# Performance work log

Hardware: AMD Instinct MI355X
Metric: run time of the kernel (lower is better)

The kernel has to match this reference:

```python
import jax, jax.numpy as jnp
import numpy as np

K = 8       # branching factor == L (max child positions)
DEPTH = 6   # tree depth
NTREE = 2   # number of trees in the forest
C = 8       # hidden states
MSYM = 32   # output symbols
NGEN = 16   # parallel generative models


def _build_tree():
    starts = [(K ** d - 1) // (K - 1) for d in range(DEPTH + 2)]
    Nt = starts[DEPTH + 1]
    N = NTREE * Nt
    rng = np.random.default_rng(0)
    x = rng.integers(0, MSYM, size=N).astype(np.int32)
    local = np.arange(Nt)
    pos = np.tile(np.where(local == 0, 0, (local - 1) % K).astype(np.int32), NTREE)
    batch = np.repeat(np.arange(NTREE), Nt).astype(np.int32)
    levels = {}
    for d in range(1, DEPTH + 1):
        ch = np.concatenate([t * Nt + np.arange(starts[d], starts[d + 1]) for t in range(NTREE)]).astype(np.int32)
        upa = np.concatenate([t * Nt + np.arange(starts[d - 1], starts[d]) for t in range(NTREE)]).astype(np.int32)
        levels[d] = (ch, upa)
    return x, pos, batch, levels


def setup_inputs() -> dict:
    key = jax.random.key(0)
    kA, kB, kPi, kSP = jax.random.split(key, 4)
    x, pos, batch, levels = _build_tree()
    inp = {
        'A': jax.random.normal(kA, (C, C, K, NGEN), jnp.float32) * 2.5,
        'B': jax.random.normal(kB, (C, MSYM, NGEN), jnp.float32) * 2.5,
        'Pi': jax.random.normal(kPi, (C, K, NGEN), jnp.float32) * 2.5,
        'SP': jax.random.normal(kSP, (K, NGEN), jnp.float32) * 2.5,
        'x': jnp.asarray(x),
        'pos': jnp.asarray(pos),
        'batch': jnp.asarray(batch),
        'leaves': jnp.asarray(levels[DEPTH][0]),
    }
    for d in range(1, DEPTH + 1):
        inp[f'ch{d}'] = jnp.asarray(levels[d][0])
        inp[f'upa{d}'] = jnp.asarray(levels[d][1])
    return inp


def _upward(A, B, Pi, SP, x, pos, batch, leaves, levels):
    # softmax reparameterization (matches the per-generator per-position loops)
    smA = jax.nn.softmax(A, axis=0)    # over parent state
    smB = jax.nn.softmax(B, axis=1)    # over symbols
    smPi = jax.nn.softmax(Pi, axis=0)  # over states
    smSP = jax.nn.softmax(SP, axis=0)  # over positions

    N = x.shape[0]
    beta = jnp.zeros((N, C, NGEN), smA.dtype)
    ll = jnp.zeros((N, NGEN), smA.dtype)

    # leaves: beta = Pi[:, pos] * B[:, x], normalized per node
    b_leaf = jnp.transpose(smPi[:, pos[leaves]], (1, 0, 2)) * jnp.transpose(smB[:, x[leaves]], (1, 0, 2))  # (nl,C,G)
    nu = b_leaf.sum(1)
    beta = beta.at[leaves].set(b_leaf / nu[:, None])
    ll = ll.at[leaves].set(jnp.log(nu))

    # per-position transition weighted by position prior: (L, i_parent, j_child, G)
    Mmat = smSP[:, None, None, :] * jnp.transpose(smA, (2, 0, 1, 3))

    # upward over levels, deepest first; children of each parent are contiguous
    # with column index == child position, so scatter-add == reshape + einsum
    for ch, upa in reversed(levels):
        U = upa.shape[0]
        bch = beta[ch].reshape(U, K, C, NGEN)              # (U, pos, C_child, G)
        tb = jnp.einsum('uljg,lijg->uig', bch, Mmat)       # t_beta at parents
        bl = tb * jnp.transpose(smB[:, x[upa]], (1, 0, 2)) # (U, C, G)
        nu = bl.sum(1)
        beta = beta.at[upa].set(bl / nu[:, None])
        ll = ll.at[upa].set(jnp.log(nu))

    # sum per-node log scaling factors over each tree
    return jax.ops.segment_sum(ll, batch, num_segments=NTREE)


def reference(A, B, Pi, SP, x, pos, batch, leaves, ch1, upa1, ch2, upa2, ch3, upa3, ch4, upa4, ch5, upa5, ch6, upa6):
    levels = [(ch1, upa1), (ch2, upa2), (ch3, upa3), (ch4, upa4), (ch5, upa5), (ch6, upa6)]
    return _upward(A, B, Pi, SP, x, pos, batch, leaves, levels)
```

## Files before the change

kernel.cpp:

```cpp
#include <hip/hip_runtime.h>


constexpr int NT_NODES = 299593;
constexpr int S0 = 0, S1 = 1, S2 = 9, S3 = 73, S4 = 585, S5 = 4681, S6 = 37449;

__device__ __forceinline__ unsigned bfbits(float x) {
    unsigned v = __float_as_uint(x);
    return (v + 0x7fffu + ((v >> 16) & 1u)) >> 16;
}

__device__ __forceinline__ float sel8(const float v[8], bool c0, bool c1, bool c2) {
    float a0 = c0 ? v[1] : v[0];
    float a1 = c0 ? v[3] : v[2];
    float a2 = c0 ? v[5] : v[4];
    float a3 = c0 ? v[7] : v[6];
    float b0 = c1 ? a1 : a0;
    float b1 = c1 ? a3 : a2;
    return c2 ? b1 : b0;
}

__global__ __launch_bounds__(256) void xpack(
    const int* __restrict__ x, uint4* __restrict__ rec)
{
    int pidx = blockIdx.x * 256 + threadIdx.x;
    int t = pidx >> 15, localP = pidx & 32767;
    const int base = t * NT_NODES;
    const int xb = base + S6 + localP * 8;
    unsigned d0 = 0, d1 = 0;
    #pragma unroll
    for (int l = 0; l < 4; ++l) d0 |= ((unsigned)x[xb + l]) << (8 * l);
    #pragma unroll
    for (int l = 0; l < 4; ++l) d1 |= ((unsigned)x[xb + 4 + l]) << (8 * l);
    unsigned xm = (unsigned)x[base + S5 + localP];
    unsigned xr = (unsigned)x[base + S4 + (localP >> 3)];
    unsigned x3 = (unsigned)x[base + S3 + (localP >> 6)];
    rec[pidx] = make_uint4(d0, d1, xm | (xr << 8) | (x3 << 16), 0u);
}

__global__ __launch_bounds__(256) void stage0T(
    const float* __restrict__ A, const float* __restrict__ B,
    const float* __restrict__ Pi, const float* __restrict__ SP,
    float* __restrict__ MtN, float* __restrict__ smBtN,
    unsigned* __restrict__ Tp, unsigned* __restrict__ EMp)
{
    int g = blockIdx.x;
    int tid = threadIdx.x;
    __shared__ __align__(16) float mL[512];
    __shared__ __align__(16) float bLs[256];
    __shared__ __align__(16) float piLs[64];

    float sp[8];
    {
        float mx = -1e30f;
        #pragma unroll
        for (int l = 0; l < 8; ++l) { sp[l] = SP[l * 16 + g]; mx = fmaxf(mx, sp[l]); }
        float s = 0.f;
        #pragma unroll
        for (int l = 0; l < 8; ++l) { sp[l] = __expf(sp[l] - mx); s += sp[l]; }
        float r = 1.f / s;
        #pragma unroll
        for (int l = 0; l < 8; ++l) sp[l] *= r;
    }

    if (tid < 64) {
        int j = tid & 7, l = tid >> 3;
        float a[8]; float mx = -1e30f;
        #pragma unroll
        for (int i = 0; i < 8; ++i) { a[i] = A[((i * 8 + j) * 8 + l) * 16 + g]; mx = fmaxf(mx, a[i]); }
        float s = 0.f;
        #pragma unroll
        for (int i = 0; i < 8; ++i) { a[i] = __expf(a[i] - mx); s += a[i]; }
        float scale = sp[l] / s;
        #pragma unroll
        for (int i = 0; i < 8; ++i) {
            float m = a[i] * scale;
            mL[(l * 8 + j) * 8 + i] = m;
            MtN[((g * 8 + l) * 8 + j) * 8 + i] = m;
        }
    } else if (tid < 72) {
        int c = tid - 64;
        float vv[32]; float mx = -1e30f;
        #pragma unroll
        for (int m = 0; m < 32; ++m) { vv[m] = B[(c * 32 + m) * 16 + g]; mx = fmaxf(mx, vv[m]); }
        float s = 0.f;
        #pragma unroll
        for (int m = 0; m < 32; ++m) { vv[m] = __expf(vv[m] - mx); s += vv[m]; }
        float r = 1.f / s;
        #pragma unroll
        for (int m = 0; m < 32; ++m) {
            float p = vv[m] * r;
            bLs[m * 8 + c] = p;
            smBtN[(g * 32 + m) * 8 + c] = p;
        }
    } else if (tid < 80) {
        int l = tid - 72;
        float a[8]; float mx = -1e30f;
        #pragma unroll
        for (int c = 0; c < 8; ++c) { a[c] = Pi[(c * 8 + l) * 16 + g]; mx = fmaxf(mx, a[c]); }
        float s = 0.f;
        #pragma unroll
        for (int c = 0; c < 8; ++c) { a[c] = __expf(a[c] - mx); s += a[c]; }
        float r = 1.f / s;
        #pragma unroll
        for (int c = 0; c < 8; ++c) piLs[l * 8 + c] = a[c] * r;
    }
    __syncthreads();

    {
        int m = tid & 31, l = tid >> 5;
        float pb[8]; float w = 0.f;
        #pragma unroll
        for (int c = 0; c < 8; ++c) { pb[c] = piLs[l * 8 + c] * bLs[m * 8 + c]; w += pb[c]; }
        float rw = 1.f / w;
        float t[8];
        #pragma unroll
        for (int i = 0; i < 8; ++i) t[i] = 0.f;
        #pragma unroll
        for (int c = 0; c < 8; ++c) {
            float p = pb[c];
            #pragma unroll
            for (int i = 0; i < 8; ++i) t[i] = fmaf(p, mL[(l * 8 + c) * 8 + i], t[i]);
        }
        #pragma unroll
        for (int k = 0; k < 4; ++k) {
            unsigned lo = bfbits(t[2 * k] * rw), hi = bfbits(t[2 * k + 1] * rw);
            Tp[(g * 5 + k) * 256 + tid] = lo | (hi << 16);
        }
        Tp[(g * 5 + 4) * 256 + tid] = __float_as_uint(__logf(w));
    }
    if (tid < 32) {
        #pragma unroll
        for (int k = 0; k < 4; ++k) {
            unsigned lo = bfbits(bLs[tid * 8 + 2 * k]), hi = bfbits(bLs[tid * 8 + 2 * k + 1]);
            EMp[(g * 4 + k) * 32 + tid] = lo | (hi << 16);
        }
    }
}

__global__ __launch_bounds__(256, 2) void upleaf(
    const float* __restrict__ MtN, const unsigned* __restrict__ Tp,
    const unsigned* __restrict__ EMp, const uint4* __restrict__ rec,
    float* __restrict__ lv3,
    float* __restrict__ llout)
{
    __shared__ unsigned TL[256 * 5 + 32 * 5];
    __shared__ float b4[256 * 9];
    __shared__ float llp[4];

    int bid = blockIdx.x;
    int g = bid & 15;
    int pg = bid >> 4;
    int tid = threadIdx.x;
    int wave = tid >> 6;
    int lane = tid & 63;
    int gu = __builtin_amdgcn_readfirstlane(g);
    int s = pg * 256 + tid;
    int t = (s >= 4096) ? 1 : 0;
    int localS = s - t * 4096;

    #pragma unroll
    for (int k = 0; k < 5; ++k)
        TL[tid * 5 + k] = Tp[(gu * 5 + k) * 256 + tid];
    if (tid < 32) {
        #pragma unroll
        for (int k = 0; k < 4; ++k)
            TL[1280 + tid * 5 + k] = EMp[(gu * 4 + k) * 32 + tid];
    }

    uint4 rc[8];
    {
        const uint4* rp = rec + ((size_t)t * 32768 + (size_t)localS * 8);
        #pragma unroll
        for (int u = 0; u < 8; ++u) rc[u] = rp[u];
    }
    int xr = (rc[0].z >> 8) & 255;
    int x3 = (rc[0].z >> 16) & 255;
    __syncthreads();

    float ll = 0.f;
    float bm[64];

    #pragma unroll
    for (int u = 0; u < 8; ++u) {
        int xl[8];
        xl[0] = rc[u].x & 255; xl[1] = (rc[u].x >> 8) & 255;
        xl[2] = (rc[u].x >> 16) & 255; xl[3] = rc[u].x >> 24;
        xl[4] = rc[u].y & 255; xl[5] = (rc[u].y >> 8) & 255;
        xl[6] = (rc[u].y >> 16) & 255; xl[7] = rc[u].y >> 24;
        int xm = rc[u].z & 255;

        float pa[8] = {0.f, 0.f, 0.f, 0.f, 0.f, 0.f, 0.f, 0.f};
        #pragma unroll
        for (int l = 0; l < 8; ++l) {
            int r5 = (l * 32 + xl[l]) * 5;
            unsigned u0 = TL[r5], u1 = TL[r5 + 1], u2 = TL[r5 + 2], u3 = TL[r5 + 3];
            ll += __uint_as_float(TL[r5 + 4]);
            pa[0] += __uint_as_float(u0 << 16); pa[1] += __uint_as_float(u0 & 0xffff0000u);
            pa[2] += __uint_as_float(u1 << 16); pa[3] += __uint_as_float(u1 & 0xffff0000u);
            pa[4] += __uint_as_float(u2 << 16); pa[5] += __uint_as_float(u2 & 0xffff0000u);
            pa[6] += __uint_as_float(u3 << 16); pa[7] += __uint_as_float(u3 & 0xffff0000u);
        }
        int e5 = 1280 + xm * 5;
        unsigned e0 = TL[e5], e1 = TL[e5 + 1], e2 = TL[e5 + 2], e3 = TL[e5 + 3];
        pa[0] *= __uint_as_float(e0 << 16); pa[1] *= __uint_as_float(e0 & 0xffff0000u);
        pa[2] *= __uint_as_float(e1 << 16); pa[3] *= __uint_as_float(e1 & 0xffff0000u);
        pa[4] *= __uint_as_float(e2 << 16); pa[5] *= __uint_as_float(e2 & 0xffff0000u);
        pa[6] *= __uint_as_float(e3 << 16); pa[7] *= __uint_as_float(e3 & 0xffff0000u);
        float nu = ((pa[0] + pa[1]) + (pa[2] + pa[3])) + ((pa[4] + pa[5]) + (pa[6] + pa[7]));
        ll += __logf(nu);
        float rn = __builtin_amdgcn_rcpf(nu);
        #pragma unroll
        for (int c = 0; c < 8; ++c) bm[u * 8 + c] = pa[c] * rn;
    }

    {
        float pr[8] = {0.f, 0.f, 0.f, 0.f, 0.f, 0.f, 0.f, 0.f};
        const float* Mg = MtN + (gu << 9);
        #pragma unroll
        for (int k = 0; k < 64; ++k) {
            float b = bm[k];
            #pragma unroll
            for (int i = 0; i < 8; ++i) pr[i] = fmaf(b, Mg[k * 8 + i], pr[i]);
        }
        int e5 = 1280 + xr * 5;
        unsigned e0 = TL[e5], e1 = TL[e5 + 1], e2 = TL[e5 + 2], e3 = TL[e5 + 3];
        pr[0] *= __uint_as_float(e0 << 16); pr[1] *= __uint_as_float(e0 & 0xffff0000u);
        pr[2] *= __uint_as_float(e1 << 16); pr[3] *= __uint_as_float(e1 & 0xffff0000u);
        pr[4] *= __uint_as_float(e2 << 16); pr[5] *= __uint_as_float(e2 & 0xffff0000u);
        pr[6] *= __uint_as_float(e3 << 16); pr[7] *= __uint_as_float(e3 & 0xffff0000u);
        float nur = ((pr[0] + pr[1]) + (pr[2] + pr[3])) + ((pr[4] + pr[5]) + (pr[6] + pr[7]));
        ll += __logf(nur);
        float rr = __builtin_amdgcn_rcpf(nur);
        #pragma unroll
        for (int c = 0; c < 8; ++c) b4[tid * 9 + c] = pr[c] * rr;
    }
    __syncthreads();

    {
        int o = tid >> 3, j = tid & 7;
        int s3 = pg * 32 + o;
        int t3 = (s3 >= 512) ? 1 : 0;
        float bch[8];
        #pragma unroll
        for (int l = 0; l < 8; ++l) bch[l] = b4[(o * 8 + l) * 9 + j];
        float pr[8] = {0.f, 0.f, 0.f, 0.f, 0.f, 0.f, 0.f, 0.f};
        #pragma unroll
        for (int l = 0; l < 8; ++l) {
            const float4* mp = (const float4*)(MtN + (gu << 9) + (l << 6) + (j << 3));
            float4 m0 = mp[0], m1 = mp[1];
            float b = bch[l];
            pr[0] = fmaf(b, m0.x, pr[0]); pr[1] = fmaf(b, m0.y, pr[1]);
            pr[2] = fmaf(b, m0.z, pr[2]); pr[3] = fmaf(b, m0.w, pr[3]);
            pr[4] = fmaf(b, m1.x, pr[4]); pr[5] = fmaf(b, m1.y, pr[5]);
            pr[6] = fmaf(b, m1.z, pr[6]); pr[7] = fmaf(b, m1.w, pr[7]);
        }
        #pragma unroll
        for (int m = 1; m <= 4; m <<= 1) {
            #pragma unroll
            for (int i = 0; i < 8; ++i) pr[i] += __shfl_xor(pr[i], m);
        }
        int xn = __shfl(x3, o * 8);
        int e5 = 1280 + xn * 5;
        unsigned e0 = TL[e5], e1 = TL[e5 + 1], e2 = TL[e5 + 2], e3 = TL[e5 + 3];
        pr[0] *= __uint_as_float(e0 << 16); pr[1] *= __uint_as_float(e0 & 0xffff0000u);
        pr[2] *= __uint_as_float(e1 << 16); pr[3] *= __uint_as_float(e1 & 0xffff0000u);
        pr[4] *= __uint_as_float(e2 << 16); pr[5] *= __uint_as_float(e2 & 0xffff0000u);
        pr[6] *= __uint_as_float(e3 << 16); pr[7] *= __uint_as_float(e3 & 0xffff0000u);
        float nur = ((pr[0] + pr[1]) + (pr[2] + pr[3])) + ((pr[4] + pr[5]) + (pr[6] + pr[7]));
        float rr = __builtin_amdgcn_rcpf(nur);
        if (j == 0) {
            ll += __logf(nur);
            float4* dp = (float4*)(lv3 + ((size_t)g * 1024 + s3) * 8);
            dp[0] = make_float4(pr[0] * rr, pr[1] * rr, pr[2] * rr, pr[3] * rr);
            dp[1] = make_float4(pr[4] * rr, pr[5] * rr, pr[6] * rr, pr[7] * rr);
        }
    }

    #pragma unroll
    for (int m = 1; m < 64; m <<= 1) ll += __shfl_xor(ll, m);
    if (lane == 0) llp[wave] = ll;
    __syncthreads();
    if (tid == 0) llout[gu * 32 + pg] = (llp[0] + llp[1]) + (llp[2] + llp[3]);
}

__global__ __launch_bounds__(256) void uptop(
    const float* __restrict__ MtN, const float* __restrict__ smBtN,
    const int* __restrict__ x,
    const float* __restrict__ lv3,
    const float* __restrict__ ll1,
    float* __restrict__ out)
{
    int g = blockIdx.x;
    int tid = threadIdx.x;
    __shared__ __align__(16) float bet2[128 * 8];
    __shared__ __align__(16) float bet1[16 * 8];
    __shared__ float redA[256], redB[256];

    float ll0 = 0.f, llt1 = 0.f;
    if (tid < 32) {
        float v = ll1[g * 32 + tid];
        if (tid < 16) ll0 = v; else llt1 = v;
    }

    const float* Mg = MtN + (g << 9);

    if (tid < 128) {
        int t = tid >> 6, n2 = tid & 63;
        float bch[64];
        const float4* sp = (const float4*)(lv3 + ((size_t)g * 1024 + t * 512 + n2 * 8) * 8);
        #pragma unroll
        for (int v = 0; v < 16; ++v) {
            float4 f = sp[v];
            bch[4 * v + 0] = f.x; bch[4 * v + 1] = f.y;
            bch[4 * v + 2] = f.z; bch[4 * v + 3] = f.w;
        }
        float pa[8] = {0.f, 0.f, 0.f, 0.f, 0.f, 0.f, 0.f, 0.f};
        #pragma unroll
        for (int k = 0; k < 64; ++k) {
            float b = bch[k];
            #pragma unroll
            for (int i = 0; i < 8; ++i) pa[i] = fmaf(b, Mg[k * 8 + i], pa[i]);
        }
        int x2 = x[t * NT_NODES + S2 + n2];
        const float4* ep = (const float4*)(smBtN + ((g << 5) + x2) * 8);
        float4 e0 = ep[0], e1 = ep[1];
        pa[0] *= e0.x; pa[1] *= e0.y; pa[2] *= e0.z; pa[3] *= e0.w;
        pa[4] *= e1.x; pa[5] *= e1.y; pa[6] *= e1.z; pa[7] *= e1.w;
        float nu = ((pa[0] + pa[1]) + (pa[2] + pa[3])) + ((pa[4] + pa[5]) + (pa[6] + pa[7]));
        float lg = __logf(nu);
        if (t == 0) ll0 += lg; else llt1 += lg;
        float rn = __builtin_amdgcn_rcpf(nu);
        float4* dp = (float4*)(bet2 + tid * 8);
        dp[0] = make_float4(pa[0] * rn, pa[1] * rn, pa[2] * rn, pa[3] * rn);
        dp[1] = make_float4(pa[4] * rn, pa[5] * rn, pa[6] * rn, pa[7] * rn);
    }
    __syncthreads();

    if (tid < 128) {
        int o = tid >> 3, j = tid & 7;
        int t = o >> 3, n1 = o & 7;
        bool c0 = (j & 1) != 0, c1 = (j & 2) != 0, c2 = (j & 4) != 0;
        float bch[8];
        #pragma unroll
        for (int l = 0; l < 8; ++l) bch[l] = bet2[(t * 64 + n1 * 8 + l) * 8 + j];
        float pr[8] = {0.f, 0.f, 0.f, 0.f, 0.f, 0.f, 0.f, 0.f};
        #pragma unroll
        for (int l = 0; l < 8; ++l) {
            const float4* mp = (const float4*)(MtN + (g << 9) + (l << 6) + (j << 3));
            float4 m0 = mp[0], m1 = mp[1];
            float b = bch[l];
            pr[0] = fmaf(b, m0.x, pr[0]); pr[1] = fmaf(b, m0.y, pr[1]);
            pr[2] = fmaf(b, m0.z, pr[2]); pr[3] = fmaf(b, m0.w, pr[3]);
            pr[4] = fmaf(b, m1.x, pr[4]); pr[5] = fmaf(b, m1.y, pr[5]);
            pr[6] = fmaf(b, m1.z, pr[6]); pr[7] = fmaf(b, m1.w, pr[7]);
        }
        #pragma unroll
        for (int m = 1; m <= 4; m <<= 1) {
            #pragma unroll
            for (int i = 0; i < 8; ++i) pr[i] += __shfl_xor(pr[i], m);
        }
        int x1 = x[t * NT_NODES + S1 + n1];
        const float4* ep = (const float4*)(smBtN + ((g << 5) + x1) * 8);
        float4 e0 = ep[0], e1 = ep[1];
        pr[0] *= e0.x; pr[1] *= e0.y; pr[2] *= e0.z; pr[3] *= e0.w;
        pr[4] *= e1.x; pr[5] *= e1.y; pr[6] *= e1.z; pr[7] *= e1.w;
        float nu = ((pr[0] + pr[1]) + (pr[2] + pr[3])) + ((pr[4] + pr[5]) + (pr[6] + pr[7]));
        if (j == 0) { float lg = __logf(nu); if (t == 0) ll0 += lg; else llt1 += lg; }
        float rn = __builtin_amdgcn_rcpf(nu);
        bet1[o * 8 + j] = sel8(pr, c0, c1, c2) * rn;
    }
    __syncthreads();

    if (tid < 16) {
        int t = tid >> 3, j = tid & 7;
        float bch[8];
        #pragma unroll
        for (int l = 0; l < 8; ++l) bch[l] = bet1[(t * 8 + l) * 8 + j];
        float pr[8] = {0.f, 0.f, 0.f, 0.f, 0.f, 0.f, 0.f, 0.f};
        #pragma unroll
        for (int l = 0; l < 8; ++l) {
            const float4* mp = (const float4*)(MtN + (g << 9) + (l << 6) + (j << 3));
            float4 m0 = mp[0], m1 = mp[1];
            float b = bch[l];
            pr[0] = fmaf(b, m0.x, pr[0]); pr[1] = fmaf(b, m0.y, pr[1]);
            pr[2] = fmaf(b, m0.z, pr[2]); pr[3] = fmaf(b, m0.w, pr[3]);
            pr[4] = fmaf(b, m1.x, pr[4]); pr[5] = fmaf(b, m1.y, pr[5]);
            pr[6] = fmaf(b, m1.z, pr[6]); pr[7] = fmaf(b, m1.w, pr[7]);
        }
        #pragma unroll
        for (int m = 1; m <= 4; m <<= 1) {
            #pragma unroll
            for (int i = 0; i < 8; ++i) pr[i] += __shfl_xor(pr[i], m);
        }
        int x0 = x[t * NT_NODES + S0];
        const float4* ep = (const float4*)(smBtN + ((g << 5) + x0) * 8);
        float4 e0 = ep[0], e1 = ep[1];
        pr[0] *= e0.x; pr[1] *= e0.y; pr[2] *= e0.z; pr[3] *= e0.w;
        pr[4] *= e1.x; pr[5] *= e1.y; pr[6] *= e1.z; pr[7] *= e1.w;
        float nu = ((pr[0] + pr[1]) + (pr[2] + pr[3])) + ((pr[4] + pr[5]) + (pr[6] + pr[7]));
        if (j == 0) { float lg = __logf(nu); if (t == 0) ll0 += lg; else llt1 += lg; }
    }

    redA[tid] = ll0; redB[tid] = llt1;
    __syncthreads();
    for (int step = 128; step > 0; step >>= 1) {
        if (tid < step) { redA[tid] += redA[tid + step]; redB[tid] += redB[tid + step]; }
        __syncthreads();
    }
    if (tid == 0) { out[g] = redA[0]; out[16 + g] = redB[0]; }
}

extern "C" void kernel_launch(void* const* d_in, const int* in_sizes, int n_in,
                              void* d_out, int out_size, void* d_ws, size_t ws_size,
                              hipStream_t stream)
{
    const float* A  = (const float*)d_in[0];
    const float* B  = (const float*)d_in[1];
    const float* Pi = (const float*)d_in[2];
    const float* SP = (const float*)d_in[3];
    const int*   x  = (const int*)d_in[4];

    float* ws     = (float*)d_ws;
    float* MtN    = ws;
    float* smBtN  = MtN + 8192;
    unsigned* Tp  = (unsigned*)(smBtN + 4096);
    unsigned* EMp = Tp + 20480;
    uint4* rec    = (uint4*)(EMp + 2048);
    float* lv3    = (float*)(rec + 65536);
    float* ll1    = lv3 + 131072;
    float* out    = (float*)d_out;

    stage0T<<<16, 256, 0, stream>>>(A, B, Pi, SP, MtN, smBtN, Tp, EMp);
    xpack<<<256, 256, 0, stream>>>(x, rec);
    upleaf<<<512, 256, 0, stream>>>(MtN, Tp, EMp, rec, lv3, ll1);
    uptop<<<16, 256, 0, stream>>>(MtN, smBtN, x, lv3, ll1, out);
}
```

Before: 30.66 us.

## Merge prep kernels and split level-5 work across wave pairs in upleaf

The parameter-softmax kernel and the symbol-packing kernel are fused into one launch, with block index selecting the role, which removes one kernel launch. In upleaf each level-5 parent's eight children are now split across two waves, with partial sums combined through shared memory. This halves per-thread register arrays, raises the occupancy hint to 4 blocks per CU and doubles the grid to 1024 blocks. In exchange it adds an extra barrier and shared-memory exchange, leaves half the threads idle during the level-4 step, and doubles the number of partial log-likelihoods that uptop must read.

```diff
diff --git a/kernel.cpp b/kernel.cpp
--- a/kernel.cpp
+++ b/kernel.cpp
@@ -19,32 +19,35 @@
     return c2 ? b1 : b0;
 }
 
-__global__ __launch_bounds__(256) void xpack(
-    const int* __restrict__ x, uint4* __restrict__ rec)
-{
-    int pidx = blockIdx.x * 256 + threadIdx.x;
-    int t = pidx >> 15, localP = pidx & 32767;
-    const int base = t * NT_NODES;
-    const int xb = base + S6 + localP * 8;
-    unsigned d0 = 0, d1 = 0;
-    #pragma unroll
-    for (int l = 0; l < 4; ++l) d0 |= ((unsigned)x[xb + l]) << (8 * l);
-    #pragma unroll
-    for (int l = 0; l < 4; ++l) d1 |= ((unsigned)x[xb + 4 + l]) << (8 * l);
-    unsigned xm = (unsigned)x[base + S5 + localP];
-    unsigned xr = (unsigned)x[base + S4 + (localP >> 3)];
-    unsigned x3 = (unsigned)x[base + S3 + (localP >> 6)];
-    rec[pidx] = make_uint4(d0, d1, xm | (xr << 8) | (x3 << 16), 0u);
-}
-
-__global__ __launch_bounds__(256) void stage0T(
+__global__ __launch_bounds__(256) void prep(
     const float* __restrict__ A, const float* __restrict__ B,
     const float* __restrict__ Pi, const float* __restrict__ SP,
+    const int* __restrict__ x,
     float* __restrict__ MtN, float* __restrict__ smBtN,
-    unsigned* __restrict__ Tp, unsigned* __restrict__ EMp)
+    unsigned* __restrict__ Tp, unsigned* __restrict__ EMp,
+    uint4* __restrict__ rec)
 {
-    int g = blockIdx.x;
+    int bid = blockIdx.x;
     int tid = threadIdx.x;
+
+    if (bid >= 16) {
+        int pidx = (bid - 16) * 256 + tid;
+        int t = pidx >> 15, localP = pidx & 32767;
+        const int base = t * NT_NODES;
+        const int xb = base + S6 + localP * 8;
+        unsigned d0 = 0, d1 = 0;
+        #pragma unroll
+        for (int l = 0; l < 4; ++l) d0 |= ((unsigned)x[xb + l]) << (8 * l);
+        #pragma unroll
+        for (int l = 0; l < 4; ++l) d1 |= ((unsigned)x[xb + 4 + l]) << (8 * l);
+        unsigned xm = (unsigned)x[base + S5 + localP];
+        unsigned xr = (unsigned)x[base + S4 + (localP >> 3)];
+        unsigned x3 = (unsigned)x[base + S3 + (localP >> 6)];
+        rec[pidx] = make_uint4(d0, d1, xm | (xr << 8) | (x3 << 16), 0u);
+        return;
+    }
+
+    int g = bid;
     __shared__ __align__(16) float mL[512];
     __shared__ __align__(16) float bLs[256];
     __shared__ __align__(16) float piLs[64];
@@ -137,14 +140,14 @@
     }
 }
 
-__global__ __launch_bounds__(256, 2) void upleaf(
+__global__ __launch_bounds__(256, 4) void upleaf(
     const float* __restrict__ MtN, const unsigned* __restrict__ Tp,
     const unsigned* __restrict__ EMp, const uint4* __restrict__ rec,
     float* __restrict__ lv3,
     float* __restrict__ llout)
 {
     __shared__ unsigned TL[256 * 5 + 32 * 5];
-    __shared__ float b4[256 * 9];
+    __shared__ float ex[128 * 9];
     __shared__ float llp[4];
 
     int bid = blockIdx.x;
@@ -153,8 +156,11 @@
     int tid = threadIdx.x;
     int wave = tid >> 6;
     int lane = tid & 63;
+    int half = wave & 1;
+    int pairIdx = wave >> 1;
     int gu = __builtin_amdgcn_readfirstlane(g);
-    int s = pg * 256 + tid;
+    int idx = pairIdx * 64 + lane;
+    int s = pg * 128 + idx;
     int t = (s >= 4096) ? 1 : 0;
     int localS = s - t * 4096;
 
@@ -167,21 +173,22 @@
             TL[1280 + tid * 5 + k] = EMp[(gu * 4 + k) * 32 + tid];
     }
 
-    uint4 rc[8];
+    uint4 rc[4];
     {
-        const uint4* rp = rec + ((size_t)t * 32768 + (size_t)localS * 8);
-        #pragma unroll
-        for (int u = 0; u < 8; ++u) rc[u] = rp[u];
-    }
-    int xr = (rc[0].z >> 8) & 255;
-    int x3 = (rc[0].z >> 16) & 255;
+        const uint4* rp = rec + ((size_t)t * 32768 + (size_t)localS * 8 + half * 4);
+        #pragma unroll
+        for (int u = 0; u < 4; ++u) rc[u] = rp[u];
+    }
+    unsigned meta = rc[0].z;
+    int xr = (meta >> 8) & 255;
+    unsigned x3b = (meta >> 16) & 255;
     __syncthreads();
 
     float ll = 0.f;
-    float bm[64];
+    float bm[32];
 
     #pragma unroll
-    for (int u = 0; u < 8; ++u) {
+    for (int u = 0; u < 4; ++u) {
         int xl[8];
         xl[0] = rc[u].x & 255; xl[1] = (rc[u].x >> 8) & 255;
         xl[2] = (rc[u].x >> 16) & 255; xl[3] = rc[u].x >> 24;
@@ -213,66 +220,76 @@
         for (int c = 0; c < 8; ++c) bm[u * 8 + c] = pa[c] * rn;
     }
 
+    float pr[8] = {0.f, 0.f, 0.f, 0.f, 0.f, 0.f, 0.f, 0.f};
     {
-        float pr[8] = {0.f, 0.f, 0.f, 0.f, 0.f, 0.f, 0.f, 0.f};
-        const float* Mg = MtN + (gu << 9);
-        #pragma unroll
-        for (int k = 0; k < 64; ++k) {
+        const float* Mg = MtN + (gu << 9) + (half << 8);
+        #pragma unroll
+        for (int k = 0; k < 32; ++k) {
             float b = bm[k];
             #pragma unroll
             for (int i = 0; i < 8; ++i) pr[i] = fmaf(b, Mg[k * 8 + i], pr[i]);
         }
+    }
+    if (half) {
+        #pragma unroll
+        for (int c = 0; c < 8; ++c) ex[idx * 9 + c] = pr[c];
+    }
+    __syncthreads();
+    if (!half) {
+        float tot[8];
+        #pragma unroll
+        for (int c = 0; c < 8; ++c) tot[c] = pr[c] + ex[idx * 9 + c];
         int e5 = 1280 + xr * 5;
         unsigned e0 = TL[e5], e1 = TL[e5 + 1], e2 = TL[e5 + 2], e3 = TL[e5 + 3];
-        pr[0] *= __uint_as_float(e0 << 16); pr[1] *= __uint_as_float(e0 & 0xffff0000u);
-        pr[2] *= __uint_as_float(e1 << 16); pr[3] *= __uint_as_float(e1 & 0xffff0000u);
-        pr[4] *= __uint_as_float(e2 << 16); pr[5] *= __uint_as_float(e2 & 0xffff0000u);
-        pr[6] *= __uint_as_float(e3 << 16); pr[7] *= __uint_as_float(e3 & 0xffff0000u);
-        float nur = ((pr[0] + pr[1]) + (pr[2] + pr[3])) + ((pr[4] + pr[5]) + (pr[6] + pr[7]));
+        tot[0] *= __uint_as_float(e0 << 16); tot[1] *= __uint_as_float(e0 & 0xffff0000u);
+        tot[2] *= __uint_as_float(e1 << 16); tot[3] *= __uint_as_float(e1 & 0xffff0000u);
+        tot[4] *= __uint_as_float(e2 << 16); tot[5] *= __uint_as_float(e2 & 0xffff0000u);
+        tot[6] *= __uint_as_float(e3 << 16); tot[7] *= __uint_as_float(e3 & 0xffff0000u);
+        float nur = ((tot[0] + tot[1]) + (tot[2] + tot[3])) + ((tot[4] + tot[5]) + (tot[6] + tot[7]));
         ll += __logf(nur);
         float rr = __builtin_amdgcn_rcpf(nur);
         #pragma unroll
-        for (int c = 0; c < 8; ++c) b4[tid * 9 + c] = pr[c] * rr;
-    }
-    __syncthreads();
-
-    {
+        for (int c = 0; c < 8; ++c) ex[idx * 9 + c] = tot[c] * rr;
+        ex[idx * 9 + 8] = __uint_as_float(x3b);
+    }
+    __syncthreads();
+
+    if (tid < 128) {
         int o = tid >> 3, j = tid & 7;
-        int s3 = pg * 32 + o;
-        int t3 = (s3 >= 512) ? 1 : 0;
+        int s3 = pg * 16 + o;
         float bch[8];
         #pragma unroll
-        for (int l = 0; l < 8; ++l) bch[l] = b4[(o * 8 + l) * 9 + j];
-        float pr[8] = {0.f, 0.f, 0.f, 0.f, 0.f, 0.f, 0.f, 0.f};
+        for (int l = 0; l < 8; ++l) bch[l] = ex[(o * 8 + l) * 9 + j];
+        float pr3[8] = {0.f, 0.f, 0.f, 0.f, 0.f, 0.f, 0.f, 0.f};
         #pragma unroll
         for (int l = 0; l < 8; ++l) {
             const float4* mp = (const float4*)(MtN + (gu << 9) + (l << 6) + (j << 3));
             float4 m0 = mp[0], m1 = mp[1];
             float b = bch[l];
-            pr[0] = fmaf(b, m0.x, pr[0]); pr[1] = fmaf(b, m0.y, pr[1]);
-            pr[2] = fmaf(b, m0.z, pr[2]); pr[3] = fmaf(b, m0.w, pr[3]);
-            pr[4] = fmaf(b, m1.x, pr[4]); pr[5] = fmaf(b, m1.y, pr[5]);
-            pr[6] = fmaf(b, m1.z, pr[6]); pr[7] = fmaf(b, m1.w, pr[7]);
+            pr3[0] = fmaf(b, m0.x, pr3[0]); pr3[1] = fmaf(b, m0.y, pr3[1]);
+            pr3[2] = fmaf(b, m0.z, pr3[2]); pr3[3] = fmaf(b, m0.w, pr3[3]);
+            pr3[4] = fmaf(b, m1.x, pr3[4]); pr3[5] = fmaf(b, m1.y, pr3[5]);
+            pr3[6] = fmaf(b, m1.z, pr3[6]); pr3[7] = fmaf(b, m1.w, pr3[7]);
         }
         #pragma unroll
         for (int m = 1; m <= 4; m <<= 1) {
             #pragma unroll
-            for (int i = 0; i < 8; ++i) pr[i] += __shfl_xor(pr[i], m);
-        }
-        int xn = __shfl(x3, o * 8);
+            for (int i = 0; i < 8; ++i) pr3[i] += __shfl_xor(pr3[i], m);
+        }
+        int xn = (int)__float_as_uint(ex[(o * 8) * 9 + 8]);
         int e5 = 1280 + xn * 5;
         unsigned e0 = TL[e5], e1 = TL[e5 + 1], e2 = TL[e5 + 2], e3 = TL[e5 + 3];
-        pr[0] *= __uint_as_float(e0 << 16); pr[1] *= __uint_as_float(e0 & 0xffff0000u);
-        pr[2] *= __uint_as_float(e1 << 16); pr[3] *= __uint_as_float(e1 & 0xffff0000u);
-        pr[4] *= __uint_as_float(e2 << 16); pr[5] *= __uint_as_float(e2 & 0xffff0000u);
-        pr[6] *= __uint_as_float(e3 << 16); pr[7] *= __uint_as_float(e3 & 0xffff0000u);
-        float nur = ((pr[0] + pr[1]) + (pr[2] + pr[3])) + ((pr[4] + pr[5]) + (pr[6] + pr[7]));
+        pr3[0] *= __uint_as_float(e0 << 16); pr3[1] *= __uint_as_float(e0 & 0xffff0000u);
+        pr3[2] *= __uint_as_float(e1 << 16); pr3[3] *= __uint_as_float(e1 & 0xffff0000u);
+        pr3[4] *= __uint_as_float(e2 << 16); pr3[5] *= __uint_as_float(e2 & 0xffff0000u);
+        pr3[6] *= __uint_as_float(e3 << 16); pr3[7] *= __uint_as_float(e3 & 0xffff0000u);
+        float nur = ((pr3[0] + pr3[1]) + (pr3[2] + pr3[3])) + ((pr3[4] + pr3[5]) + (pr3[6] + pr3[7]));
         float rr = __builtin_amdgcn_rcpf(nur);
         if (j == 0) {
             ll += __logf(nur);
             float4* dp = (float4*)(lv3 + ((size_t)g * 1024 + s3) * 8);
-            dp[0] = make_float4(pr[0] * rr, pr[1] * rr, pr[2] * rr, pr[3] * rr);
-            dp[1] = make_float4(pr[4] * rr, pr[5] * rr, pr[6] * rr, pr[7] * rr);
+            dp[0] = make_float4(pr3[0] * rr, pr3[1] * rr, pr3[2] * rr, pr3[3] * rr);
+            dp[1] = make_float4(pr3[4] * rr, pr3[5] * rr, pr3[6] * rr, pr3[7] * rr);
         }
     }
 
@@ -280,7 +297,7 @@
     for (int m = 1; m < 64; m <<= 1) ll += __shfl_xor(ll, m);
     if (lane == 0) llp[wave] = ll;
     __syncthreads();
-    if (tid == 0) llout[gu * 32 + pg] = (llp[0] + llp[1]) + (llp[2] + llp[3]);
+    if (tid == 0) llout[gu * 64 + pg] = (llp[0] + llp[1]) + (llp[2] + llp[3]);
 }
 
 __global__ __launch_bounds__(256) void uptop(
@@ -297,9 +314,9 @@
     __shared__ float redA[256], redB[256];
 
     float ll0 = 0.f, llt1 = 0.f;
-    if (tid < 32) {
-        float v = ll1[g * 32 + tid];
-        if (tid < 16) ll0 = v; else llt1 = v;
+    if (tid < 64) {
+        float v = ll1[g * 64 + tid];
+        if (tid < 32) ll0 = v; else llt1 = v;
     }
 
     const float* Mg = MtN + (g << 9);
@@ -430,8 +447,7 @@
     float* ll1    = lv3 + 131072;
     float* out    = (float*)d_out;
 
-    stage0T<<<16, 256, 0, stream>>>(A, B, Pi, SP, MtN, smBtN, Tp, EMp);
-    xpack<<<256, 256, 0, stream>>>(x, rec);
-    upleaf<<<512, 256, 0, stream>>>(MtN, Tp, EMp, rec, lv3, ll1);
+    prep<<<272, 256, 0, stream>>>(A, B, Pi, SP, x, MtN, smBtN, Tp, EMp, rec);
+    upleaf<<<1024, 256, 0, stream>>>(MtN, Tp, EMp, rec, lv3, ll1);
     uptop<<<16, 256, 0, stream>>>(MtN, smBtN, x, lv3, ll1, out);
 }
```

Result: faster. 29.81 us (median of 3 runs) (-2.8%).
